# Optimization experiments

Measured on AMD Instinct MI355X. Metric: run time of the kernel, lower is better.

## Reference

```python
import jax, jax.numpy as jnp
import numpy as np

B, N, F_IN, H, E, C = 64, 1024, 128, 128, 1048576, 6
RATIO = 0.5
N1 = int(N * RATIO)        # nodes per graph after pool1 = 512
N2 = int(N1 * RATIO)       # nodes per graph after pool2 = 256


def setup_inputs() -> dict:
    key = jax.random.key(0)
    ks = jax.random.split(key, 14)
    x = jax.random.normal(ks[0], (B * N, F_IN), jnp.float32)
    # edges constrained within each graph (uniform graph size N)
    src = jax.random.randint(ks[1], (E,), 0, B * N, dtype=jnp.int32)
    dst = (src // N) * N + jax.random.randint(ks[2], (E,), 0, N, dtype=jnp.int32)
    edge_index = jnp.stack([src, dst]).astype(jnp.int64)
    batch = jnp.repeat(jnp.arange(B, dtype=jnp.int64), N)

    def lin(k, i, o):
        return (jax.random.normal(k, (i, o), jnp.float32) / np.sqrt(i)).astype(jnp.float32)

    W1 = lin(ks[3], F_IN, H); b1 = jnp.zeros((H,), jnp.float32)
    ws1 = jax.random.normal(ks[4], (H,), jnp.float32) / np.sqrt(H)
    W2 = lin(ks[5], H, H); b2 = jnp.zeros((H,), jnp.float32)
    ws2 = jax.random.normal(ks[6], (H,), jnp.float32) / np.sqrt(H)
    W3 = lin(ks[7], H, H); b3 = jnp.zeros((H,), jnp.float32)
    ws3 = jax.random.normal(ks[8], (H,), jnp.float32) / np.sqrt(H)
    L1w = lin(ks[9], 2 * H, H); L1b = jnp.zeros((H,), jnp.float32)
    L2w = lin(ks[10], H, H // 2); L2b = jnp.zeros((H // 2,), jnp.float32)
    L3w = lin(ks[11], H // 2, C); L3b = jnp.zeros((C,), jnp.float32)
    return dict(x=x, edge_index=edge_index, batch=batch,
                W1=W1, b1=b1, ws1=ws1, W2=W2, b2=b2, ws2=ws2, W3=W3, b3=b3, ws3=ws3,
                L1w=L1w, L1b=L1b, L2w=L2w, L2b=L2b, L3w=L3w, L3b=L3b)


def gcn_conv(x, src, dst, emask, W, b, ws, n_nodes):
    # GCNConv with self-loops: out_i = sum_j m_ij h_j / sqrt(d_i d_j) + h_i / d_i, d = deg+1
    h = x @ W
    deg = jax.ops.segment_sum(emask, dst, num_segments=n_nodes) + 1.0
    norm = emask / jnp.sqrt(deg[src] * deg[dst])                 # [E]
    agg = jax.ops.segment_sum(h[src] * norm[:, None], dst, num_segments=n_nodes)
    out = agg + h / deg[:, None] + b
    score = out @ ws                                             # [n] attention score
    return out, score


def att_pool(x, score, src, dst, emask, n_per_graph):
    # top-k node selection per graph (uniform sizes -> static shapes)
    k = int(n_per_graph * RATIO)
    vals, idx = jax.lax.top_k(score.reshape(B, n_per_graph), k)  # [B, k]
    gidx = (idx + (jnp.arange(B) * n_per_graph)[:, None]).reshape(-1)
    x_new = x[gidx] * jnp.tanh(vals.reshape(-1))[:, None]
    # remap old node ids -> new compact ids; drop edges touching removed nodes
    newpos = jnp.full((B * n_per_graph,), -1, jnp.int32).at[gidx].set(
        jnp.arange(B * k, dtype=jnp.int32))
    nsrc = newpos[src]; ndst = newpos[dst]
    nmask = emask * (nsrc >= 0) * (ndst >= 0)
    return x_new, jnp.maximum(nsrc, 0), jnp.maximum(ndst, 0), nmask, k


def readout(h, bvec, n_per_graph):
    gmp = jax.ops.segment_max(h, bvec, num_segments=B)
    gap = jax.ops.segment_sum(h, bvec, num_segments=B) / n_per_graph
    return jnp.concatenate([gmp, gap], axis=1)                   # [B, 2H]


def reference(x, edge_index, batch, W1, b1, ws1, W2, b2, ws2, W3, b3, ws3,
              L1w, L1b, L2w, L2b, L3w, L3b):
    src = edge_index[0].astype(jnp.int32)
    dst = edge_index[1].astype(jnp.int32)
    emask = jnp.ones((E,), x.dtype)

    h, s = gcn_conv(x, src, dst, emask, W1, b1, ws1, B * N)
    h = jax.nn.relu(h)
    h, src, dst, emask, k1 = att_pool(h, s, src, dst, emask, N)
    b1v = jnp.repeat(jnp.arange(B), k1)
    x1 = readout(h, b1v, float(k1))

    h, s = gcn_conv(h, src, dst, emask, W2, b2, ws2, B * k1)
    h = jax.nn.relu(h)
    h, src, dst, emask, k2 = att_pool(h, s, src, dst, emask, k1)
    b2v = jnp.repeat(jnp.arange(B), k2)
    x2 = readout(h, b2v, float(k2))

    h, s = gcn_conv(h, src, dst, emask, W3, b3, ws3, B * k2)
    h = jax.nn.relu(h)
    x3 = readout(h, b2v, float(k2))

    z = jax.nn.relu(x1) + jax.nn.relu(x2) + jax.nn.relu(x3)
    z = jax.nn.relu(z @ L1w + L1b)
    z = jax.nn.relu(z @ L2w + L2b)
    return jax.nn.log_softmax(z @ L3w + L3b, axis=-1)
```

## Files before the change

### kernel.cpp

```cpp
#include <hip/hip_runtime.h>
#include <math.h>

#define E_TOT 1048576
#define NB    64
#define HD    128
#define NN1   65536
#define NN2   32768
#define NN3   16384
#define CAP   18432
#define WST   140
#define PSTR  64

__global__ void probe_kernel(const int* __restrict__ ei, int* __restrict__ flag,
                             int* __restrict__ gcur, int2* __restrict__ csr2) {
    int t = threadIdx.x;
    if (t < 64) { gcur[t] = 0; csr2[E_TOT + t] = make_int2(0, 0); }
    if (blockIdx.x == 0 && t == 0) {
        int w = 1;
        for (int i = 1; i < 64; i += 2) if (ei[i] != 0) { w = 0; break; }
        *flag = w;
    }
}

__global__ __launch_bounds__(256) void bin_pack_kernel(const int* __restrict__ ei,
                                                       const int* __restrict__ wflag,
                                                       int* __restrict__ bins,
                                                       int* __restrict__ gcur) {
    __shared__ int hist[64];
    __shared__ int base[64];
    __shared__ int gpos[64];
    __shared__ int stage[4096];
    const int t = threadIdx.x;
    const int wide = *wflag;
    const int e0 = blockIdx.x * 4096;
    const int2* ei2 = (const int2*)ei;

    int pk[16];
    #pragma unroll
    for (int j = 0; j < 16; ++j) {
        int e = e0 + j * 256 + t;
        int s, d;
        if (wide) { s = ei2[e].x; d = ei2[E_TOT + e].x; }
        else      { s = ei[e];    d = ei[E_TOT + e]; }
        int g = d >> 10;
        pk[j] = (g << 20) | ((d & 1023) << 10) | (s & 1023);
    }
    if (t < 64) hist[t] = 0;
    __syncthreads();
    #pragma unroll
    for (int j = 0; j < 16; ++j) atomicAdd(&hist[pk[j] >> 20], 1);
    __syncthreads();
    if (t < 64) {
        int v = hist[t];
        int inc = v;
        #pragma unroll
        for (int d = 1; d < 64; d <<= 1) { int u = __shfl_up(inc, d); if (t >= d) inc += u; }
        base[t] = inc - v;
        gpos[t] = atomicAdd(&gcur[t], v);
    }
    __syncthreads();
    if (t < 64) hist[t] = base[t];
    __syncthreads();
    #pragma unroll
    for (int j = 0; j < 16; ++j) {
        int p = atomicAdd(&hist[pk[j] >> 20], 1);
        stage[p] = pk[j];
    }
    __syncthreads();
    #pragma unroll
    for (int j = 0; j < 16; ++j) {
        int i = j * 256 + t;
        int v = stage[i];
        int g = v >> 20;
        int dst = gpos[g] + (i - base[g]);
        if (dst < CAP) bins[g * CAP + dst] = v;
    }
}

__global__ __launch_bounds__(1024) void graph_csr_kernel(const int* __restrict__ bins,
                                                         const int* __restrict__ gcur,
                                                         int2* __restrict__ off2,
                                                         float* __restrict__ rs,
                                                         int2* __restrict__ csr2,
                                                         int* __restrict__ perm) {
    __shared__ int   deg[1024];
    __shared__ int   cur[1024];
    __shared__ float rsl[1024];
    __shared__ int   wsum[16];
    __shared__ int   dh[64];
    __shared__ int   dc[64];
    __shared__ int   ebase_s;
    const int g = blockIdx.x, t = threadIdx.x;
    const int lane = t & 63, wv = t >> 6;

    if (t < 64) {
        int v = gcur[t];
        int inc = v;
        #pragma unroll
        for (int d = 1; d < 64; d <<= 1) { int u = __shfl_up(inc, d); if (t >= d) inc += u; }
        if (t == g) ebase_s = inc - v;
    }
    deg[t] = 0;
    if (t < 64) dh[t] = 0;
    __syncthreads();
    const int cnt = gcur[g];
    const int ebase = ebase_s;
    const int* bin = bins + g * CAP;

    for (int i = t; i < cnt; i += 1024)
        atomicAdd(&deg[(bin[i] >> 10) & 1023], 1);
    __syncthreads();

    int dv = deg[t];
    int dcap = dv < 63 ? dv : 63;
    atomicAdd(&dh[dcap], 1);
    int inc = dv;
    #pragma unroll
    for (int d = 1; d < 64; d <<= 1) { int u = __shfl_up(inc, d); if (lane >= d) inc += u; }
    if (lane == 63) wsum[wv] = inc;
    __syncthreads();
    if (t < 16) {
        int v = wsum[t];
        int inc2 = v;
        #pragma unroll
        for (int d = 1; d < 16; d <<= 1) { int u = __shfl_up(inc2, d); if (t >= d) inc2 += u; }
        wsum[t] = inc2 - v;
    }
    if (t >= 64 && t < 128) {
        int l2 = t - 64;
        int v2 = dh[l2];
        int inc3 = v2;
        #pragma unroll
        for (int d = 1; d < 64; d <<= 1) { int u = __shfl_up(inc3, d); if (l2 >= d) inc3 += u; }
        dc[l2] = inc3 - v2;
    }
    __syncthreads();
    int ex = inc - dv + wsum[wv];
    int beg = ebase + ex;
    off2[g * 1024 + t] = make_int2(beg, beg + dv);
    float rv = rsqrtf((float)(dv + 1));
    rs[g * 1024 + t] = rv;
    rsl[t] = rv;
    cur[t] = ex;
    int r2 = atomicAdd(&dc[dcap], 1);
    perm[g * 1024 + r2] = t;
    __syncthreads();

    for (int i = t; i < cnt; i += 1024) {
        int v = bin[i];
        int s = v & 1023;
        int d = (v >> 10) & 1023;
        int p = atomicAdd(&cur[d], 1);
        csr2[ebase + p] = make_int2((g << 10) + s, __float_as_int(rsl[s] * rsl[d]));
    }
}

__global__ __launch_bounds__(256) void csr_build_kernel(const int2* __restrict__ old_off2,
                                                        const int* __restrict__ old_deg,
                                                        const int* __restrict__ old_csr,
                                                        int old_stride,
                                                        const int* __restrict__ map,
                                                        const int* __restrict__ sel,
                                                        int* __restrict__ new_csr,
                                                        int* __restrict__ deg,
                                                        float* __restrict__ rs, int nnew) {
    int wid  = (blockIdx.x * blockDim.x + threadIdx.x) >> 6;
    int lane = threadIdx.x & 63;
    if (wid >= nnew) return;
    int old = sel[wid];
    int beg, end;
    if (old_off2) { int2 oe = old_off2[old]; beg = oe.x; end = oe.y; }
    else          { beg = old * PSTR; end = beg + old_deg[old]; }
    int out = wid * PSTR;
    int total = 0;
    for (int base = beg; base < end; base += 64) {
        int i = base + lane;
        int ns = -1;
        if (i < end) ns = map[old_csr[i * old_stride]];
        unsigned long long b = __ballot(ns >= 0);
        int pos = __popcll(b & ((1ULL << lane) - 1));
        if (ns >= 0 && total + pos < PSTR) new_csr[out + total + pos] = ns;
        total += __popcll(b);
    }
    if (total > PSTR) total = PSTR;
    if (lane == 0) {
        deg[wid] = total;
        rs[wid]  = rsqrtf((float)(total + 1));
    }
}

__global__ __launch_bounds__(256) void gemm_tiled_kernel(const float* __restrict__ X,
                                                         const float* __restrict__ W,
                                                         float* __restrict__ Y) {
    __shared__ float sXT[2][16][128];
    __shared__ float sW[2][16][WST];
    const int t = threadIdx.x;
    const long long row0 = (long long)blockIdx.x * 128;
    const int r0 = (t >> 4) << 3;
    const int c0 = (t & 15) << 3;
    const int wofs = c0 + ((c0 >> 5) << 2);
    const int lm  = t >> 1;
    const int lk  = (t & 1) << 3;
    const int wk  = t >> 4;
    const int wc8 = (t & 15) << 3;
    const int wpos = wc8 + ((wc8 >> 5) << 2);

    float acc[8][8];
    #pragma unroll
    for (int i = 0; i < 8; ++i)
        #pragma unroll
        for (int j = 0; j < 8; ++j) acc[i][j] = 0.f;

    {
        float4 xa = *(const float4*)(X + (row0 + lm) * 128 + lk);
        float4 xb = *(const float4*)(X + (row0 + lm) * 128 + lk + 4);
        float4 wa = *(const float4*)(W + wk * 128 + wc8);
        float4 wb = *(const float4*)(W + wk * 128 + wc8 + 4);
        sXT[0][lk + 0][lm] = xa.x; sXT[0][lk + 1][lm] = xa.y;
        sXT[0][lk + 2][lm] = xa.z; sXT[0][lk + 3][lm] = xa.w;
        sXT[0][lk + 4][lm] = xb.x; sXT[0][lk + 5][lm] = xb.y;
        sXT[0][lk + 6][lm] = xb.z; sXT[0][lk + 7][lm] = xb.w;
        *(float4*)&sW[0][wk][wpos]     = wa;
        *(float4*)&sW[0][wk][wpos + 4] = wb;
    }
    int cur = 0;
    for (int k0 = 0; k0 < 128; k0 += 16) {
        __syncthreads();
        const bool hasNext = (k0 + 16) < 128;
        float4 nxa, nxb, nwa, nwb;
        if (hasNext) {
            nxa = *(const float4*)(X + (row0 + lm) * 128 + k0 + 16 + lk);
            nxb = *(const float4*)(X + (row0 + lm) * 128 + k0 + 16 + lk + 4);
            nwa = *(const float4*)(W + (k0 + 16 + wk) * 128 + wc8);
            nwb = *(const float4*)(W + (k0 + 16 + wk) * 128 + wc8 + 4);
        }
        #pragma unroll
        for (int kk = 0; kk < 16; ++kk) {
            float4 xa = *(const float4*)&sXT[cur][kk][r0];
            float4 xb = *(const float4*)&sXT[cur][kk][r0 + 4];
            float4 wa = *(const float4*)&sW[cur][kk][wofs];
            float4 wb = *(const float4*)&sW[cur][kk][wofs + 4];
            float xr[8]  = {xa.x, xa.y, xa.z, xa.w, xb.x, xb.y, xb.z, xb.w};
            float wcv[8] = {wa.x, wa.y, wa.z, wa.w, wb.x, wb.y, wb.z, wb.w};
            #pragma unroll
            for (int i = 0; i < 8; ++i)
                #pragma unroll
                for (int j = 0; j < 8; ++j)
                    acc[i][j] = fmaf(xr[i], wcv[j], acc[i][j]);
        }
        if (hasNext) {
            int nxt = cur ^ 1;
            sXT[nxt][lk + 0][lm] = nxa.x; sXT[nxt][lk + 1][lm] = nxa.y;
            sXT[nxt][lk + 2][lm] = nxa.z; sXT[nxt][lk + 3][lm] = nxa.w;
            sXT[nxt][lk + 4][lm] = nxb.x; sXT[nxt][lk + 5][lm] = nxb.y;
            sXT[nxt][lk + 6][lm] = nxb.z; sXT[nxt][lk + 7][lm] = nxb.w;
            *(float4*)&sW[nxt][wk][wpos]     = nwa;
            *(float4*)&sW[nxt][wk][wpos + 4] = nwb;
            cur = nxt;
        }
    }

    #pragma unroll
    for (int i = 0; i < 8; ++i) {
        float* yp = Y + (row0 + r0 + i) * 128 + c0;
        float4 o0; o0.x = acc[i][0]; o0.y = acc[i][1]; o0.z = acc[i][2]; o0.w = acc[i][3];
        float4 o1; o1.x = acc[i][4]; o1.y = acc[i][5]; o1.z = acc[i][6]; o1.w = acc[i][7];
        *(float4*)yp       = o0;
        *(float4*)(yp + 4) = o1;
    }
}

__global__ __launch_bounds__(256) void gemm_gather_kernel(const float* __restrict__ H,
                                                          const int* __restrict__ sel,
                                                          const float* __restrict__ scal,
                                                          const float* __restrict__ W,
                                                          float* __restrict__ Y) {
    __shared__ float sXT[2][16][128];
    __shared__ float sW[2][16][WST];
    const int t = threadIdx.x;
    const long long row0 = (long long)blockIdx.x * 128;
    const int r0 = (t >> 4) << 3;
    const int c0 = (t & 15) << 3;
    const int wofs = c0 + ((c0 >> 5) << 2);
    const int lm  = t >> 1;
    const int lk  = (t & 1) << 3;
    const int wk  = t >> 4;
    const int wc8 = (t & 15) << 3;
    const int wpos = wc8 + ((wc8 >> 5) << 2);

    const float* xrow = H + (long long)sel[row0 + lm] * 128;
    const float  sc   = scal[row0 + lm];

    float acc[8][8];
    #pragma unroll
    for (int i = 0; i < 8; ++i)
        #pragma unroll
        for (int j = 0; j < 8; ++j) acc[i][j] = 0.f;

    {
        float4 xa = *(const float4*)(xrow + lk);
        float4 xb = *(const float4*)(xrow + lk + 4);
        float4 wa = *(const float4*)(W + wk * 128 + wc8);
        float4 wb = *(const float4*)(W + wk * 128 + wc8 + 4);
        sXT[0][lk + 0][lm] = xa.x * sc; sXT[0][lk + 1][lm] = xa.y * sc;
        sXT[0][lk + 2][lm] = xa.z * sc; sXT[0][lk + 3][lm] = xa.w * sc;
        sXT[0][lk + 4][lm] = xb.x * sc; sXT[0][lk + 5][lm] = xb.y * sc;
        sXT[0][lk + 6][lm] = xb.z * sc; sXT[0][lk + 7][lm] = xb.w * sc;
        *(float4*)&sW[0][wk][wpos]     = wa;
        *(float4*)&sW[0][wk][wpos + 4] = wb;
    }
    int cur = 0;
    for (int k0 = 0; k0 < 128; k0 += 16) {
        __syncthreads();
        const bool hasNext = (k0 + 16) < 128;
        float4 nxa, nxb, nwa, nwb;
        if (hasNext) {
            nxa = *(const float4*)(xrow + k0 + 16 + lk);
            nxb = *(const float4*)(xrow + k0 + 16 + lk + 4);
            nwa = *(const float4*)(W + (k0 + 16 + wk) * 128 + wc8);
            nwb = *(const float4*)(W + (k0 + 16 + wk) * 128 + wc8 + 4);
        }
        #pragma unroll
        for (int kk = 0; kk < 16; ++kk) {
            float4 xa = *(const float4*)&sXT[cur][kk][r0];
            float4 xb = *(const float4*)&sXT[cur][kk][r0 + 4];
            float4 wa = *(const float4*)&sW[cur][kk][wofs];
            float4 wb = *(const float4*)&sW[cur][kk][wofs + 4];
            float xr[8]  = {xa.x, xa.y, xa.z, xa.w, xb.x, xb.y, xb.z, xb.w};
            float wcv[8] = {wa.x, wa.y, wa.z, wa.w, wb.x, wb.y, wb.z, wb.w};
            #pragma unroll
            for (int i = 0; i < 8; ++i)
                #pragma unroll
                for (int j = 0; j < 8; ++j)
                    acc[i][j] = fmaf(xr[i], wcv[j], acc[i][j]);
        }
        if (hasNext) {
            int nxt = cur ^ 1;
            sXT[nxt][lk + 0][lm] = nxa.x * sc; sXT[nxt][lk + 1][lm] = nxa.y * sc;
            sXT[nxt][lk + 2][lm] = nxa.z * sc; sXT[nxt][lk + 3][lm] = nxa.w * sc;
            sXT[nxt][lk + 4][lm] = nxb.x * sc; sXT[nxt][lk + 5][lm] = nxb.y * sc;
            sXT[nxt][lk + 6][lm] = nxb.z * sc; sXT[nxt][lk + 7][lm] = nxb.w * sc;
            *(float4*)&sW[nxt][wk][wpos]     = nwa;
            *(float4*)&sW[nxt][wk][wpos + 4] = nwb;
            cur = nxt;
        }
    }

    #pragma unroll
    for (int i = 0; i < 8; ++i) {
        float* yp = Y + (row0 + r0 + i) * 128 + c0;
        float4 o0; o0.x = acc[i][0]; o0.y = acc[i][1]; o0.z = acc[i][2]; o0.w = acc[i][3];
        float4 o1; o1.x = acc[i][4]; o1.y = acc[i][5]; o1.z = acc[i][6]; o1.w = acc[i][7];
        *(float4*)yp       = o0;
        *(float4*)(yp + 4) = o1;
    }
}

__global__ __launch_bounds__(1024) void agg_lds_kernel(const float* __restrict__ h,
                                                       const int2* __restrict__ csr2,
                                                       const int2* __restrict__ off2,
                                                       const float* __restrict__ rs,
                                                       const int* __restrict__ perm,
                                                       const float* __restrict__ bias,
                                                       const float* __restrict__ ws,
                                                       float* __restrict__ hrelu,
                                                       float* __restrict__ P) {
    __shared__ float sh[1024 * 36];
    const int t  = threadIdx.x;
    const int g  = blockIdx.x & 63;
    const int fc = blockIdx.x >> 6;
    const int nbase = g << 10;
    const float* hg = h + (size_t)nbase * 128 + fc * 32;

    #pragma unroll
    for (int it = 0; it < 8; ++it) {
        int i = it * 1024 + t;
        int r = i >> 3, p = i & 7;
        float4 v4 = *(const float4*)(hg + (size_t)r * 128 + p * 4);
        *(float4*)&sh[r * 36 + p * 4] = v4;
    }
    __syncthreads();

    const int q   = t & 7;
    const int grp = t >> 3;
    const int qb  = q << 2;

    float4 bb = *(const float4*)(bias + fc * 32 + qb);
    float4 ww = *(const float4*)(ws   + fc * 32 + qb);

    for (int pass = 0; pass < 8; ++pass) {
        int lv = perm[nbase + pass * 128 + grp];
        int v  = nbase + lv;
        int2 oe = off2[v];
        int beg = oe.x, end = oe.y;
        float rv = rs[v];
        float a0 = 0.f, a1 = 0.f, a2 = 0.f, a3 = 0.f;

        int2 er = csr2[beg + q];
        for (int eb = beg; eb < end; eb += 8) {
            int2 ern = csr2[eb + 8 + q];
            #pragma unroll
            for (int j = 0; j < 8; ++j) {
                int   sj = __shfl(er.x, j, 8);
                float nr = __int_as_float(__shfl(er.y, j, 8));
                float nj = (eb + j < end) ? nr : 0.f;
                const float4 e = *(const float4*)&sh[(sj & 1023) * 36 + qb];
                a0 = fmaf(e.x, nj, a0); a1 = fmaf(e.y, nj, a1);
                a2 = fmaf(e.z, nj, a2); a3 = fmaf(e.w, nj, a3);
            }
            er = ern;
        }

        float4 hv = *(const float4*)&sh[lv * 36 + qb];
        float inv = rv * rv;
        float o0 = a0 + hv.x * inv + bb.x;
        float o1 = a1 + hv.y * inv + bb.y;
        float o2 = a2 + hv.z * inv + bb.z;
        float o3 = a3 + hv.w * inv + bb.w;

        float pa = o0 * ww.x + o1 * ww.y;
        float pb = o2 * ww.z + o3 * ww.w;
        *(float2*)(P + (size_t)v * 64 + (fc * 8 + q) * 2) = make_float2(pa, pb);

        float4 o;
        o.x = fmaxf(o0, 0.f); o.y = fmaxf(o1, 0.f);
        o.z = fmaxf(o2, 0.f); o.w = fmaxf(o3, 0.f);
        *(float4*)(hrelu + (size_t)v * 128 + fc * 32 + qb) = o;
    }
}

__global__ __launch_bounds__(256) void score1_kernel(const float* __restrict__ P,
                                                     float* __restrict__ score) {
    int v = blockIdx.x * 256 + threadIdx.x;
    const float* buf = P + (size_t)v * 64;
    float a[32], b[32];
    #pragma unroll
    for (int i2 = 0; i2 < 16; ++i2) {
        float4 v4 = *(const float4*)(buf + i2 * 4);
        a[i2 * 2]     = v4.x; b[i2 * 2]     = v4.y;
        a[i2 * 2 + 1] = v4.z; b[i2 * 2 + 1] = v4.w;
    }
    float ua[16], ub[16];
    #pragma unroll
    for (int l = 0; l < 16; ++l) { ua[l] = a[l] + a[l + 16]; ub[l] = b[l] + b[l + 16]; }
    float va[8], vb[8];
    #pragma unroll
    for (int l = 0; l < 8; ++l) { va[l] = ua[l] + ua[l + 8]; vb[l] = ub[l] + ub[l + 8]; }
    float wa[4], wb[4];
    #pragma unroll
    for (int l = 0; l < 4; ++l) { wa[l] = va[l] + va[l + 4]; wb[l] = vb[l] + vb[l + 4]; }
    float xa0 = wa[0] + wa[2], xa1 = wa[1] + wa[3];
    float xb0 = wb[0] + wb[2], xb1 = wb[1] + wb[3];
    score[v] = (xa0 + xa1) + (xb0 + xb1);
}

__global__ __launch_bounds__(256) void agg_kernel(const float* __restrict__ h,
                                                  const int* __restrict__ csr,
                                                  const int2* __restrict__ off2,
                                                  const int* __restrict__ degp,
                                                  const float* __restrict__ rs,
                                                  const float* __restrict__ bias,
                                                  const float* __restrict__ ws,
                                                  float* __restrict__ hrelu,
                                                  float* __restrict__ score,
                                                  int npg, int lbshift, int padded) {
    const int lane = threadIdx.x & 63;
    const int wvb  = threadIdx.x >> 6;
    const int half = lane >> 5;
    const int li   = lane & 31;
    int b   = blockIdx.x;
    int xcd = b & 7;
    int i   = b >> 3;
    int gi  = i >> lbshift;
    int lb  = i & ((1 << lbshift) - 1);
    int g   = xcd + (gi << 3);
    int v   = g * npg + (lb << 3) + (wvb << 1) + half;

    int beg, end;
    if (padded) { beg = v * PSTR; end = beg + degp[v]; }
    else        { int2 oe = off2[v]; beg = oe.x; end = oe.y; }
    float rv = rs[v];
    const float4* h4 = (const float4*)h;
    float ax = 0.f, ay = 0.f, az = 0.f, aw = 0.f;

    for (int base = beg; base < end; base += 32) {
        int idx = base + li;
        int sv = (idx < end) ? csr[idx] : 0;
        int m = end - base; if (m > 32) m = 32;
        int j = 0;
        for (; j + 8 <= m; j += 8) {
            int s0 = __shfl(sv, j,     32);
            int s1 = __shfl(sv, j + 1, 32);
            int s2 = __shfl(sv, j + 2, 32);
            int s3 = __shfl(sv, j + 3, 32);
            int s4 = __shfl(sv, j + 4, 32);
            int s5 = __shfl(sv, j + 5, 32);
            int s6 = __shfl(sv, j + 6, 32);
            int s7 = __shfl(sv, j + 7, 32);
            float n0 = rs[s0] * rv, n1 = rs[s1] * rv, n2 = rs[s2] * rv, n3 = rs[s3] * rv;
            float n4 = rs[s4] * rv, n5 = rs[s5] * rv, n6 = rs[s6] * rv, n7 = rs[s7] * rv;
            float4 v0 = h4[(long long)s0 * 32 + li];
            float4 v1 = h4[(long long)s1 * 32 + li];
            float4 v2 = h4[(long long)s2 * 32 + li];
            float4 v3 = h4[(long long)s3 * 32 + li];
            float4 v4 = h4[(long long)s4 * 32 + li];
            float4 v5 = h4[(long long)s5 * 32 + li];
            float4 v6 = h4[(long long)s6 * 32 + li];
            float4 v7 = h4[(long long)s7 * 32 + li];
            ax = fmaf(v0.x, n0, ax); ay = fmaf(v0.y, n0, ay); az = fmaf(v0.z, n0, az); aw = fmaf(v0.w, n0, aw);
            ax = fmaf(v1.x, n1, ax); ay = fmaf(v1.y, n1, ay); az = fmaf(v1.z, n1, az); aw = fmaf(v1.w, n1, aw);
            ax = fmaf(v2.x, n2, ax); ay = fmaf(v2.y, n2, ay); az = fmaf(v2.z, n2, az); aw = fmaf(v2.w, n2, aw);
            ax = fmaf(v3.x, n3, ax); ay = fmaf(v3.y, n3, ay); az = fmaf(v3.z, n3, az); aw = fmaf(v3.w, n3, aw);
            ax = fmaf(v4.x, n4, ax); ay = fmaf(v4.y, n4, ay); az = fmaf(v4.z, n4, az); aw = fmaf(v4.w, n4, aw);
            ax = fmaf(v5.x, n5, ax); ay = fmaf(v5.y, n5, ay); az = fmaf(v5.z, n5, az); aw = fmaf(v5.w, n5, aw);
            ax = fmaf(v6.x, n6, ax); ay = fmaf(v6.y, n6, ay); az = fmaf(v6.z, n6, az); aw = fmaf(v6.w, n6, aw);
            ax = fmaf(v7.x, n7, ax); ay = fmaf(v7.y, n7, ay); az = fmaf(v7.z, n7, az); aw = fmaf(v7.w, n7, aw);
        }
        for (; j < m; ++j) {
            int s = __shfl(sv, j, 32);
            float n = rs[s] * rv;
            float4 vv = h4[(long long)s * 32 + li];
            ax = fmaf(vv.x, n, ax); ay = fmaf(vv.y, n, ay);
            az = fmaf(vv.z, n, az); aw = fmaf(vv.w, n, aw);
        }
    }

    float4 hv = h4[(long long)v * 32 + li];
    float inv = rv * rv;
    float4 bb = ((const float4*)bias)[li];
    float4 ww = ((const float4*)ws)[li];
    float o0 = ax + hv.x * inv + bb.x;
    float o1 = ay + hv.y * inv + bb.y;
    float o2 = az + hv.z * inv + bb.z;
    float o3 = aw + hv.w * inv + bb.w;

    float pa = o0 * ww.x + o1 * ww.y;
    float pb = o2 * ww.z + o3 * ww.w;
    #pragma unroll
    for (int dd = 16; dd; dd >>= 1) {
        pa += __shfl_xor(pa, dd, 32);
        pb += __shfl_xor(pb, dd, 32);
    }
    float p = pa + pb;
    if (li == 0) score[v] = p;

    float4 o;
    o.x = fmaxf(o0, 0.f); o.y = fmaxf(o1, 0.f);
    o.z = fmaxf(o2, 0.f); o.w = fmaxf(o3, 0.f);
    ((float4*)hrelu)[(long long)v * 32 + li] = o;
}

__global__ __launch_bounds__(1024) void topk_kernel(const float* __restrict__ score,
                                                    int* __restrict__ newpos,
                                                    int* __restrict__ sel,
                                                    float* __restrict__ scale,
                                                    int n, int k) {
    __shared__ float key[1024];
    __shared__ int   kid[1024];
    int g = blockIdx.x, t = threadIdx.x;
    key[t] = score[g * n + t];
    kid[t] = t;
    __syncthreads();
    for (int kk = 2; kk <= n; kk <<= 1) {
        for (int j = kk >> 1; j > 0; j >>= 1) {
            int ixj = t ^ j;
            if (ixj > t) {
                bool dir = ((t & kk) == 0);
                float a = key[t], b = key[ixj];
                if ((a < b) == dir) {
                    key[t] = b; key[ixj] = a;
                    int tmp = kid[t]; kid[t] = kid[ixj]; kid[ixj] = tmp;
                }
            }
            __syncthreads();
        }
    }
    int old = g * n + kid[t];
    if (t < k) {
        int nid = g * k + t;
        newpos[old] = nid;
        sel[nid]    = old;
        scale[nid]  = tanhf(key[t]);
    } else {
        newpos[old] = -1;
    }
}

__global__ __launch_bounds__(128) void readout_part_kernel(const float* __restrict__ h,
                                                           float* __restrict__ part, int npg) {
    int b = blockIdx.x;
    int g = b >> 3, c = b & 7;
    int f = threadIdx.x;
    int chunk = npg >> 3;
    const float* base = h + ((long long)g * npg + (long long)c * chunk) * 128;
    float m = -INFINITY, s = 0.f;
    for (int n = 0; n < chunk; ++n) {
        float v = base[n * 128 + f];
        m = fmaxf(m, v);
        s += v;
    }
    part[(size_t)b * 256 + f]       = m;
    part[(size_t)b * 256 + 128 + f] = s;
}

__global__ __launch_bounds__(128) void readout_gpart_kernel(const float* __restrict__ h,
                                                            const int* __restrict__ sel,
                                                            const float* __restrict__ scal,
                                                            float* __restrict__ part, int npg) {
    int b = blockIdx.x;
    int g = b >> 3, c = b & 7;
    int f = threadIdx.x;
    int chunk = npg >> 3;
    int i0 = g * npg + c * chunk;
    float m = -INFINITY, s = 0.f;
    for (int n = 0; n < chunk; ++n) {
        int idx = i0 + n;
        float v = h[(long long)sel[idx] * 128 + f] * scal[idx];
        m = fmaxf(m, v);
        s += v;
    }
    part[(size_t)b * 256 + f]       = m;
    part[(size_t)b * 256 + 128 + f] = s;
}

__global__ __launch_bounds__(128) void mlp_kernel(const float* __restrict__ part1,
                                                  const float* __restrict__ part2,
                                                  const float* __restrict__ part3,
                                                  const float* __restrict__ L1w,
                                                  const float* __restrict__ L1b,
                                                  const float* __restrict__ L2w,
                                                  const float* __restrict__ L2b,
                                                  const float* __restrict__ L3w,
                                                  const float* __restrict__ L3b,
                                                  float* __restrict__ out) {
    __shared__ float z[256], z1[128], z2[64], z3[6];
    int g = blockIdx.x, t = threadIdx.x;
    float m1 = -INFINITY, s1 = 0.f, m2 = -INFINITY, s2 = 0.f, m3 = -INFINITY, s3 = 0.f;
    #pragma unroll
    for (int c = 0; c < 8; ++c) {
        size_t o = (size_t)(g * 8 + c) * 256;
        m1 = fmaxf(m1, part1[o + t]); s1 += part1[o + 128 + t];
        m2 = fmaxf(m2, part2[o + t]); s2 += part2[o + 128 + t];
        m3 = fmaxf(m3, part3[o + t]); s3 += part3[o + 128 + t];
    }
    z[t]       = fmaxf(m1, 0.f) + fmaxf(m2, 0.f) + fmaxf(m3, 0.f);
    z[t + 128] = fmaxf(s1 / 512.f, 0.f) + fmaxf(s2 / 256.f, 0.f) + fmaxf(s3 / 256.f, 0.f);
    __syncthreads();
    float a = L1b[t];
    for (int i = 0; i < 256; ++i) a += z[i] * L1w[i * 128 + t];
    z1[t] = fmaxf(a, 0.f);
    __syncthreads();
    if (t < 64) {
        float b = L2b[t];
        for (int i = 0; i < 128; ++i) b += z1[i] * L2w[i * 64 + t];
        z2[t] = fmaxf(b, 0.f);
    }
    __syncthreads();
    if (t < 6) {
        float c = L3b[t];
        for (int i = 0; i < 64; ++i) c += z2[i] * L3w[i * 6 + t];
        z3[t] = c;
    }
    __syncthreads();
    if (t == 0) {
        float m = z3[0];
        for (int i = 1; i < 6; ++i) m = fmaxf(m, z3[i]);
        float s = 0.f;
        for (int i = 0; i < 6; ++i) s += expf(z3[i] - m);
        float ls = m + logf(s);
        for (int i = 0; i < 6; ++i) out[g * 6 + i] = z3[i] - ls;
    }
}

extern "C" void kernel_launch(void* const* d_in, const int* in_sizes, int n_in,
                              void* d_out, int out_size, void* d_ws, size_t ws_size,
                              hipStream_t stream) {
    const float* x    = (const float*)d_in[0];
    const int*   ei   = (const int*)d_in[1];
    const float* W1   = (const float*)d_in[3];
    const float* b1   = (const float*)d_in[4];
    const float* ws1  = (const float*)d_in[5];
    const float* W2   = (const float*)d_in[6];
    const float* b2   = (const float*)d_in[7];
    const float* ws2  = (const float*)d_in[8];
    const float* W3   = (const float*)d_in[9];
    const float* b3   = (const float*)d_in[10];
    const float* ws3  = (const float*)d_in[11];
    const float* L1w  = (const float*)d_in[12];
    const float* L1b  = (const float*)d_in[13];
    const float* L2w  = (const float*)d_in[14];
    const float* L2b  = (const float*)d_in[15];
    const float* L3w  = (const float*)d_in[16];
    const float* L3b  = (const float*)d_in[17];
    float* out = (float*)d_out;

    char* w = (char*)d_ws;
    auto alloc = [&](size_t nbytes) { char* p = w; w += (nbytes + 255) & ~(size_t)255; return p; };
    float* A     = (float*)alloc((size_t)NN1 * 128 * 4);
    float* Bf    = (float*)alloc((size_t)NN1 * 128 * 4);
    float* P1    = (float*)alloc((size_t)NN1 * 64 * 4);
    float* P2    = (float*)alloc((size_t)NN3 * 128 * 4);
    int2*  csr2  = (int2*)alloc((size_t)(E_TOT + 64) * 8);
    int*   degA  = (int*)alloc((size_t)NN2 * 4);
    int*   degB  = (int*)alloc((size_t)NN3 * 4);
    int2*  off2A = (int2*)alloc((size_t)NN1 * 8);
    float* rs    = (float*)alloc((size_t)NN1 * 4);
    int*   perm  = (int*)alloc((size_t)NN1 * 4);
    int*   np1   = (int*)alloc((size_t)NN1 * 4);
    int*   np2   = (int*)alloc((size_t)NN2 * 4);
    int*   sel   = (int*)alloc((size_t)NN2 * 4);
    float* scal  = (float*)alloc((size_t)NN2 * 4);
    float* score = (float*)alloc((size_t)NN1 * 4);
    float* part1 = (float*)alloc((size_t)NB * 8 * 256 * 4);
    float* part2 = (float*)alloc((size_t)NB * 8 * 256 * 4);
    float* part3 = (float*)alloc((size_t)NB * 8 * 256 * 4);
    int*   gcur  = (int*)alloc(64 * 4);
    int*   flag  = (int*)alloc(256);

    int*   bins = (int*)P2;
    float* Pp   = P1;
    int*   csrB = (int*)P1;
    int*   csrC = (int*)csr2;

    probe_kernel<<<1, 64, 0, stream>>>(ei, flag, gcur, csr2);

    bin_pack_kernel<<<E_TOT / 4096, 256, 0, stream>>>(ei, flag, bins, gcur);
    graph_csr_kernel<<<NB, 1024, 0, stream>>>(bins, gcur, off2A, rs, csr2, perm);
    gemm_tiled_kernel<<<NN1 / 128, 256, 0, stream>>>(x, W1, A);
    agg_lds_kernel<<<256, 1024, 0, stream>>>(A, csr2, off2A, rs, perm, b1, ws1, Bf, Pp);
    score1_kernel<<<NN1 / 256, 256, 0, stream>>>(Pp, score);
    topk_kernel<<<NB, 1024, 0, stream>>>(score, np1, sel, scal, 1024, 512);
    readout_gpart_kernel<<<NB * 8, 128, 0, stream>>>(Bf, sel, scal, part1, 512);

    csr_build_kernel<<<NN2 / 4, 256, 0, stream>>>(off2A, nullptr, (const int*)csr2, 2,
                                                  np1, sel, csrB, degA, rs, NN2);
    gemm_gather_kernel<<<NN2 / 128, 256, 0, stream>>>(Bf, sel, scal, W2, A);
    agg_kernel<<<NN2 / 8, 256, 0, stream>>>(A, csrB, nullptr, degA, rs, b2, ws2,
                                            Bf, score, 512, 6, 1);
    topk_kernel<<<NB, 512, 0, stream>>>(score, np2, sel, scal, 512, 256);
    readout_gpart_kernel<<<NB * 8, 128, 0, stream>>>(Bf, sel, scal, part2, 256);

    csr_build_kernel<<<NN3 / 4, 256, 0, stream>>>(nullptr, degA, csrB, 1,
                                                  np2, sel, csrC, degB, rs, NN3);
    gemm_gather_kernel<<<NN3 / 128, 256, 0, stream>>>(Bf, sel, scal, W3, A);
    agg_kernel<<<NN3 / 8, 256, 0, stream>>>(A, csrC, nullptr, degB, rs, b3, ws3,
                                            Bf, score, 256, 5, 1);
    readout_part_kernel<<<NB * 8, 128, 0, stream>>>(Bf, part3, 256);

    mlp_kernel<<<NB, 128, 0, stream>>>(part1, part2, part3, L1w, L1b, L2w, L2b,
                                       L3w, L3b, out);
}
```

Baseline: 360.0 us.

## Fuse independent stage kernels into block-partitioned launches and simplify edge loop

Merges independent kernels into single launches that dispatch on block index: bin packing plus the first GEMM, and per-stage gather-GEMM, CSR rebuild and readout. Shared memory is now dynamic and carved per role. This removes several kernel launches and the serialization between independent work, so they can run concurrently on the GPU. The first-layer aggregation loop also drops the shuffle-based prefetch of edges in favour of direct loads with a separate tail, which may change memory latency hiding. The fused kernels use the largest role's shared memory and registers for every block, which could lower occupancy for the lighter roles.

```diff
diff --git a/kernel.cpp b/kernel.cpp
--- a/kernel.cpp
+++ b/kernel.cpp
@@ -10,6 +10,7 @@
 #define CAP   18432
 #define WST   140
 #define PSTR  64
+#define SMEM_PREP (2*16*128*4 + 2*16*WST*4)
 
 __global__ void probe_kernel(const int* __restrict__ ei, int* __restrict__ flag,
                              int* __restrict__ gcur, int2* __restrict__ csr2) {
@@ -22,17 +23,17 @@
     }
 }
 
-__global__ __launch_bounds__(256) void bin_pack_kernel(const int* __restrict__ ei,
-                                                       const int* __restrict__ wflag,
-                                                       int* __restrict__ bins,
-                                                       int* __restrict__ gcur) {
-    __shared__ int hist[64];
-    __shared__ int base[64];
-    __shared__ int gpos[64];
-    __shared__ int stage[4096];
+__device__ __forceinline__ void bin_pack_body(char* smem, const int* __restrict__ ei,
+                                              const int* __restrict__ wflag,
+                                              int* __restrict__ bins,
+                                              int* __restrict__ gcur, int bid) {
+    int* hist  = (int*)smem;
+    int* base  = hist + 64;
+    int* gpos  = base + 64;
+    int* stage = gpos + 64;
     const int t = threadIdx.x;
     const int wide = *wflag;
-    const int e0 = blockIdx.x * 4096;
+    const int e0 = bid * 4096;
     const int2* ei2 = (const int2*)ei;
 
     int pk[16];
@@ -75,6 +76,186 @@
         int dst = gpos[g] + (i - base[g]);
         if (dst < CAP) bins[g * CAP + dst] = v;
     }
+}
+
+__device__ __forceinline__ void gemm_body(char* smem, const float* __restrict__ X,
+                                          const int* __restrict__ sel,
+                                          const float* __restrict__ scal,
+                                          const float* __restrict__ W,
+                                          float* __restrict__ Y, int bid) {
+    float* sXT = (float*)smem;
+    float* sW  = sXT + 2 * 16 * 128;
+    const int t = threadIdx.x;
+    const long long row0 = (long long)bid * 128;
+    const int r0 = (t >> 4) << 3;
+    const int c0 = (t & 15) << 3;
+    const int wofs = c0 + ((c0 >> 5) << 2);
+    const int lm  = t >> 1;
+    const int lk  = (t & 1) << 3;
+    const int wk  = t >> 4;
+    const int wc8 = (t & 15) << 3;
+    const int wpos = wc8 + ((wc8 >> 5) << 2);
+
+    const float* xrow;
+    float sc;
+    if (sel) { xrow = X + (long long)sel[row0 + lm] * 128; sc = scal[row0 + lm]; }
+    else     { xrow = X + (row0 + lm) * 128;               sc = 1.f; }
+
+    float acc[8][8];
+    #pragma unroll
+    for (int i = 0; i < 8; ++i)
+        #pragma unroll
+        for (int j = 0; j < 8; ++j) acc[i][j] = 0.f;
+
+    {
+        float4 xa = *(const float4*)(xrow + lk);
+        float4 xb = *(const float4*)(xrow + lk + 4);
+        float4 wa = *(const float4*)(W + wk * 128 + wc8);
+        float4 wb = *(const float4*)(W + wk * 128 + wc8 + 4);
+        sXT[(lk + 0) * 128 + lm] = xa.x * sc; sXT[(lk + 1) * 128 + lm] = xa.y * sc;
+        sXT[(lk + 2) * 128 + lm] = xa.z * sc; sXT[(lk + 3) * 128 + lm] = xa.w * sc;
+        sXT[(lk + 4) * 128 + lm] = xb.x * sc; sXT[(lk + 5) * 128 + lm] = xb.y * sc;
+        sXT[(lk + 6) * 128 + lm] = xb.z * sc; sXT[(lk + 7) * 128 + lm] = xb.w * sc;
+        *(float4*)&sW[wk * WST + wpos]     = wa;
+        *(float4*)&sW[wk * WST + wpos + 4] = wb;
+    }
+    int cur = 0;
+    for (int k0 = 0; k0 < 128; k0 += 16) {
+        __syncthreads();
+        const bool hasNext = (k0 + 16) < 128;
+        float4 nxa, nxb, nwa, nwb;
+        if (hasNext) {
+            nxa = *(const float4*)(xrow + k0 + 16 + lk);
+            nxb = *(const float4*)(xrow + k0 + 16 + lk + 4);
+            nwa = *(const float4*)(W + (k0 + 16 + wk) * 128 + wc8);
+            nwb = *(const float4*)(W + (k0 + 16 + wk) * 128 + wc8 + 4);
+        }
+        #pragma unroll
+        for (int kk = 0; kk < 16; ++kk) {
+            float4 xa = *(const float4*)&sXT[(cur * 16 + kk) * 128 + r0];
+            float4 xb = *(const float4*)&sXT[(cur * 16 + kk) * 128 + r0 + 4];
+            float4 wa = *(const float4*)&sW[(cur * 16 + kk) * WST + wofs];
+            float4 wb = *(const float4*)&sW[(cur * 16 + kk) * WST + wofs + 4];
+            float xr[8]  = {xa.x, xa.y, xa.z, xa.w, xb.x, xb.y, xb.z, xb.w};
+            float wcv[8] = {wa.x, wa.y, wa.z, wa.w, wb.x, wb.y, wb.z, wb.w};
+            #pragma unroll
+            for (int i = 0; i < 8; ++i)
+                #pragma unroll
+                for (int j = 0; j < 8; ++j)
+                    acc[i][j] = fmaf(xr[i], wcv[j], acc[i][j]);
+        }
+        if (hasNext) {
+            int nxt = cur ^ 1;
+            sXT[(nxt * 16 + lk + 0) * 128 + lm] = nxa.x * sc;
+            sXT[(nxt * 16 + lk + 1) * 128 + lm] = nxa.y * sc;
+            sXT[(nxt * 16 + lk + 2) * 128 + lm] = nxa.z * sc;
+            sXT[(nxt * 16 + lk + 3) * 128 + lm] = nxa.w * sc;
+            sXT[(nxt * 16 + lk + 4) * 128 + lm] = nxb.x * sc;
+            sXT[(nxt * 16 + lk + 5) * 128 + lm] = nxb.y * sc;
+            sXT[(nxt * 16 + lk + 6) * 128 + lm] = nxb.z * sc;
+            sXT[(nxt * 16 + lk + 7) * 128 + lm] = nxb.w * sc;
+            *(float4*)&sW[(nxt * 16 + wk) * WST + wpos]     = nwa;
+            *(float4*)&sW[(nxt * 16 + wk) * WST + wpos + 4] = nwb;
+            cur = nxt;
+        }
+    }
+
+    #pragma unroll
+    for (int i = 0; i < 8; ++i) {
+        float* yp = Y + (row0 + r0 + i) * 128 + c0;
+        float4 o0; o0.x = acc[i][0]; o0.y = acc[i][1]; o0.z = acc[i][2]; o0.w = acc[i][3];
+        float4 o1; o1.x = acc[i][4]; o1.y = acc[i][5]; o1.z = acc[i][6]; o1.w = acc[i][7];
+        *(float4*)yp       = o0;
+        *(float4*)(yp + 4) = o1;
+    }
+}
+
+__device__ __forceinline__ void csr_build_body(const int2* __restrict__ old_off2,
+                                               const int* __restrict__ old_deg,
+                                               const int* __restrict__ old_csr,
+                                               int old_stride,
+                                               const int* __restrict__ map,
+                                               const int* __restrict__ sel,
+                                               int* __restrict__ new_csr,
+                                               int* __restrict__ deg,
+                                               float* __restrict__ rs,
+                                               int nnew, int wid, int lane) {
+    if (wid >= nnew) return;
+    int old = sel[wid];
+    int beg, end;
+    if (old_off2) { int2 oe = old_off2[old]; beg = oe.x; end = oe.y; }
+    else          { beg = old * PSTR; end = beg + old_deg[old]; }
+    int out = wid * PSTR;
+    int total = 0;
+    for (int base = beg; base < end; base += 64) {
+        int i = base + lane;
+        int ns = -1;
+        if (i < end) ns = map[old_csr[i * old_stride]];
+        unsigned long long b = __ballot(ns >= 0);
+        int pos = __popcll(b & ((1ULL << lane) - 1));
+        if (ns >= 0 && total + pos < PSTR) new_csr[out + total + pos] = ns;
+        total += __popcll(b);
+    }
+    if (total > PSTR) total = PSTR;
+    if (lane == 0) {
+        deg[wid] = total;
+        rs[wid]  = rsqrtf((float)(total + 1));
+    }
+}
+
+__device__ __forceinline__ void readout_g_body(const float* __restrict__ h,
+                                               const int* __restrict__ sel,
+                                               const float* __restrict__ scal,
+                                               float* __restrict__ part,
+                                               int npg, int b, int f) {
+    int g = b >> 3, c = b & 7;
+    int chunk = npg >> 3;
+    int i0 = g * npg + c * chunk;
+    float m = -INFINITY, s = 0.f;
+    for (int n = 0; n < chunk; ++n) {
+        int idx = i0 + n;
+        float v = h[(long long)sel[idx] * 128 + f] * scal[idx];
+        m = fmaxf(m, v);
+        s += v;
+    }
+    part[(size_t)b * 256 + f]       = m;
+    part[(size_t)b * 256 + 128 + f] = s;
+}
+
+__global__ __launch_bounds__(256) void prep1_kernel(const int* __restrict__ ei,
+                                                    const int* __restrict__ wflag,
+                                                    int* __restrict__ bins,
+                                                    int* __restrict__ gcur,
+                                                    const float* __restrict__ X,
+                                                    const float* __restrict__ W1,
+                                                    float* __restrict__ A) {
+    extern __shared__ __align__(16) char smem[];
+    if (blockIdx.x < 256) bin_pack_body(smem, ei, wflag, bins, gcur, blockIdx.x);
+    else                  gemm_body(smem, X, nullptr, nullptr, W1, A, blockIdx.x - 256);
+}
+
+__global__ __launch_bounds__(256) void stage_prep_kernel(
+        const float* __restrict__ Bf, const int* __restrict__ sel,
+        const float* __restrict__ scal, const float* __restrict__ W,
+        float* __restrict__ A,
+        const int2* __restrict__ old_off2, const int* __restrict__ old_deg,
+        const int* __restrict__ old_csr, int old_stride,
+        const int* __restrict__ map, int* __restrict__ new_csr,
+        int* __restrict__ deg, float* __restrict__ rs, int nnew,
+        float* __restrict__ part, int npg, int ngemm, int ncsr) {
+    extern __shared__ __align__(16) char smem[];
+    int b = blockIdx.x;
+    if (b < ngemm) { gemm_body(smem, Bf, sel, scal, W, A, b); return; }
+    b -= ngemm;
+    if (b < ncsr) {
+        csr_build_body(old_off2, old_deg, old_csr, old_stride, map, sel,
+                       new_csr, deg, rs, nnew, b * 4 + (threadIdx.x >> 6),
+                       threadIdx.x & 63);
+        return;
+    }
+    b -= ncsr;
+    readout_g_body(Bf, sel, scal, part, npg, b * 2 + (threadIdx.x >> 7),
+                   threadIdx.x & 127);
 }
 
 __global__ __launch_bounds__(1024) void graph_csr_kernel(const int* __restrict__ bins,
@@ -155,207 +336,6 @@
     }
 }
 
-__global__ __launch_bounds__(256) void csr_build_kernel(const int2* __restrict__ old_off2,
-                                                        const int* __restrict__ old_deg,
-                                                        const int* __restrict__ old_csr,
-                                                        int old_stride,
-                                                        const int* __restrict__ map,
-                                                        const int* __restrict__ sel,
-                                                        int* __restrict__ new_csr,
-                                                        int* __restrict__ deg,
-                                                        float* __restrict__ rs, int nnew) {
-    int wid  = (blockIdx.x * blockDim.x + threadIdx.x) >> 6;
-    int lane = threadIdx.x & 63;
-    if (wid >= nnew) return;
-    int old = sel[wid];
-    int beg, end;
-    if (old_off2) { int2 oe = old_off2[old]; beg = oe.x; end = oe.y; }
-    else          { beg = old * PSTR; end = beg + old_deg[old]; }
-    int out = wid * PSTR;
-    int total = 0;
-    for (int base = beg; base < end; base += 64) {
-        int i = base + lane;
-        int ns = -1;
-        if (i < end) ns = map[old_csr[i * old_stride]];
-        unsigned long long b = __ballot(ns >= 0);
-        int pos = __popcll(b & ((1ULL << lane) - 1));
-        if (ns >= 0 && total + pos < PSTR) new_csr[out + total + pos] = ns;
-        total += __popcll(b);
-    }
-    if (total > PSTR) total = PSTR;
-    if (lane == 0) {
-        deg[wid] = total;
-        rs[wid]  = rsqrtf((float)(total + 1));
-    }
-}
-
-__global__ __launch_bounds__(256) void gemm_tiled_kernel(const float* __restrict__ X,
-                                                         const float* __restrict__ W,
-                                                         float* __restrict__ Y) {
-    __shared__ float sXT[2][16][128];
-    __shared__ float sW[2][16][WST];
-    const int t = threadIdx.x;
-    const long long row0 = (long long)blockIdx.x * 128;
-    const int r0 = (t >> 4) << 3;
-    const int c0 = (t & 15) << 3;
-    const int wofs = c0 + ((c0 >> 5) << 2);
-    const int lm  = t >> 1;
-    const int lk  = (t & 1) << 3;
-    const int wk  = t >> 4;
-    const int wc8 = (t & 15) << 3;
-    const int wpos = wc8 + ((wc8 >> 5) << 2);
-
-    float acc[8][8];
-    #pragma unroll
-    for (int i = 0; i < 8; ++i)
-        #pragma unroll
-        for (int j = 0; j < 8; ++j) acc[i][j] = 0.f;
-
-    {
-        float4 xa = *(const float4*)(X + (row0 + lm) * 128 + lk);
-        float4 xb = *(const float4*)(X + (row0 + lm) * 128 + lk + 4);
-        float4 wa = *(const float4*)(W + wk * 128 + wc8);
-        float4 wb = *(const float4*)(W + wk * 128 + wc8 + 4);
-        sXT[0][lk + 0][lm] = xa.x; sXT[0][lk + 1][lm] = xa.y;
-        sXT[0][lk + 2][lm] = xa.z; sXT[0][lk + 3][lm] = xa.w;
-        sXT[0][lk + 4][lm] = xb.x; sXT[0][lk + 5][lm] = xb.y;
-        sXT[0][lk + 6][lm] = xb.z; sXT[0][lk + 7][lm] = xb.w;
-        *(float4*)&sW[0][wk][wpos]     = wa;
-        *(float4*)&sW[0][wk][wpos + 4] = wb;
-    }
-    int cur = 0;
-    for (int k0 = 0; k0 < 128; k0 += 16) {
-        __syncthreads();
-        const bool hasNext = (k0 + 16) < 128;
-        float4 nxa, nxb, nwa, nwb;
-        if (hasNext) {
-            nxa = *(const float4*)(X + (row0 + lm) * 128 + k0 + 16 + lk);
-            nxb = *(const float4*)(X + (row0 + lm) * 128 + k0 + 16 + lk + 4);
-            nwa = *(const float4*)(W + (k0 + 16 + wk) * 128 + wc8);
-            nwb = *(const float4*)(W + (k0 + 16 + wk) * 128 + wc8 + 4);
-        }
-        #pragma unroll
-        for (int kk = 0; kk < 16; ++kk) {
-            float4 xa = *(const float4*)&sXT[cur][kk][r0];
-            float4 xb = *(const float4*)&sXT[cur][kk][r0 + 4];
-            float4 wa = *(const float4*)&sW[cur][kk][wofs];
-            float4 wb = *(const float4*)&sW[cur][kk][wofs + 4];
-            float xr[8]  = {xa.x, xa.y, xa.z, xa.w, xb.x, xb.y, xb.z, xb.w};
-            float wcv[8] = {wa.x, wa.y, wa.z, wa.w, wb.x, wb.y, wb.z, wb.w};
-            #pragma unroll
-            for (int i = 0; i < 8; ++i)
-                #pragma unroll
-                for (int j = 0; j < 8; ++j)
-                    acc[i][j] = fmaf(xr[i], wcv[j], acc[i][j]);
-        }
-        if (hasNext) {
-            int nxt = cur ^ 1;
-            sXT[nxt][lk + 0][lm] = nxa.x; sXT[nxt][lk + 1][lm] = nxa.y;
-            sXT[nxt][lk + 2][lm] = nxa.z; sXT[nxt][lk + 3][lm] = nxa.w;
-            sXT[nxt][lk + 4][lm] = nxb.x; sXT[nxt][lk + 5][lm] = nxb.y;
-            sXT[nxt][lk + 6][lm] = nxb.z; sXT[nxt][lk + 7][lm] = nxb.w;
-            *(float4*)&sW[nxt][wk][wpos]     = nwa;
-            *(float4*)&sW[nxt][wk][wpos + 4] = nwb;
-            cur = nxt;
-        }
-    }
-
-    #pragma unroll
-    for (int i = 0; i < 8; ++i) {
-        float* yp = Y + (row0 + r0 + i) * 128 + c0;
-        float4 o0; o0.x = acc[i][0]; o0.y = acc[i][1]; o0.z = acc[i][2]; o0.w = acc[i][3];
-        float4 o1; o1.x = acc[i][4]; o1.y = acc[i][5]; o1.z = acc[i][6]; o1.w = acc[i][7];
-        *(float4*)yp       = o0;
-        *(float4*)(yp + 4) = o1;
-    }
-}
-
-__global__ __launch_bounds__(256) void gemm_gather_kernel(const float* __restrict__ H,
-                                                          const int* __restrict__ sel,
-                                                          const float* __restrict__ scal,
-                                                          const float* __restrict__ W,
-                                                          float* __restrict__ Y) {
-    __shared__ float sXT[2][16][128];
-    __shared__ float sW[2][16][WST];
-    const int t = threadIdx.x;
-    const long long row0 = (long long)blockIdx.x * 128;
-    const int r0 = (t >> 4) << 3;
-    const int c0 = (t & 15) << 3;
-    const int wofs = c0 + ((c0 >> 5) << 2);
-    const int lm  = t >> 1;
-    const int lk  = (t & 1) << 3;
-    const int wk  = t >> 4;
-    const int wc8 = (t & 15) << 3;
-    const int wpos = wc8 + ((wc8 >> 5) << 2);
-
-    const float* xrow = H + (long long)sel[row0 + lm] * 128;
-    const float  sc   = scal[row0 + lm];
-
-    float acc[8][8];
-    #pragma unroll
-    for (int i = 0; i < 8; ++i)
-        #pragma unroll
-        for (int j = 0; j < 8; ++j) acc[i][j] = 0.f;
-
-    {
-        float4 xa = *(const float4*)(xrow + lk);
-        float4 xb = *(const float4*)(xrow + lk + 4);
-        float4 wa = *(const float4*)(W + wk * 128 + wc8);
-        float4 wb = *(const float4*)(W + wk * 128 + wc8 + 4);
-        sXT[0][lk + 0][lm] = xa.x * sc; sXT[0][lk + 1][lm] = xa.y * sc;
-        sXT[0][lk + 2][lm] = xa.z * sc; sXT[0][lk + 3][lm] = xa.w * sc;
-        sXT[0][lk + 4][lm] = xb.x * sc; sXT[0][lk + 5][lm] = xb.y * sc;
-        sXT[0][lk + 6][lm] = xb.z * sc; sXT[0][lk + 7][lm] = xb.w * sc;
-        *(float4*)&sW[0][wk][wpos]     = wa;
-        *(float4*)&sW[0][wk][wpos + 4] = wb;
-    }
-    int cur = 0;
-    for (int k0 = 0; k0 < 128; k0 += 16) {
-        __syncthreads();
-        const bool hasNext = (k0 + 16) < 128;
-        float4 nxa, nxb, nwa, nwb;
-        if (hasNext) {
-            nxa = *(const float4*)(xrow + k0 + 16 + lk);
-            nxb = *(const float4*)(xrow + k0 + 16 + lk + 4);
-            nwa = *(const float4*)(W + (k0 + 16 + wk) * 128 + wc8);
-            nwb = *(const float4*)(W + (k0 + 16 + wk) * 128 + wc8 + 4);
-        }
-        #pragma unroll
-        for (int kk = 0; kk < 16; ++kk) {
-            float4 xa = *(const float4*)&sXT[cur][kk][r0];
-            float4 xb = *(const float4*)&sXT[cur][kk][r0 + 4];
-            float4 wa = *(const float4*)&sW[cur][kk][wofs];
-            float4 wb = *(const float4*)&sW[cur][kk][wofs + 4];
-            float xr[8]  = {xa.x, xa.y, xa.z, xa.w, xb.x, xb.y, xb.z, xb.w};
-            float wcv[8] = {wa.x, wa.y, wa.z, wa.w, wb.x, wb.y, wb.z, wb.w};
-            #pragma unroll
-            for (int i = 0; i < 8; ++i)
-                #pragma unroll
-                for (int j = 0; j < 8; ++j)
-                    acc[i][j] = fmaf(xr[i], wcv[j], acc[i][j]);
-        }
-        if (hasNext) {
-            int nxt = cur ^ 1;
-            sXT[nxt][lk + 0][lm] = nxa.x * sc; sXT[nxt][lk + 1][lm] = nxa.y * sc;
-            sXT[nxt][lk + 2][lm] = nxa.z * sc; sXT[nxt][lk + 3][lm] = nxa.w * sc;
-            sXT[nxt][lk + 4][lm] = nxb.x * sc; sXT[nxt][lk + 5][lm] = nxb.y * sc;
-            sXT[nxt][lk + 6][lm] = nxb.z * sc; sXT[nxt][lk + 7][lm] = nxb.w * sc;
-            *(float4*)&sW[nxt][wk][wpos]     = nwa;
-            *(float4*)&sW[nxt][wk][wpos + 4] = nwb;
-            cur = nxt;
-        }
-    }
-
-    #pragma unroll
-    for (int i = 0; i < 8; ++i) {
-        float* yp = Y + (row0 + r0 + i) * 128 + c0;
-        float4 o0; o0.x = acc[i][0]; o0.y = acc[i][1]; o0.z = acc[i][2]; o0.w = acc[i][3];
-        float4 o1; o1.x = acc[i][4]; o1.y = acc[i][5]; o1.z = acc[i][6]; o1.w = acc[i][7];
-        *(float4*)yp       = o0;
-        *(float4*)(yp + 4) = o1;
-    }
-}
-
 __global__ __launch_bounds__(1024) void agg_lds_kernel(const float* __restrict__ h,
                                                        const int2* __restrict__ csr2,
                                                        const int2* __restrict__ off2,
@@ -396,19 +376,26 @@
         float rv = rs[v];
         float a0 = 0.f, a1 = 0.f, a2 = 0.f, a3 = 0.f;
 
-        int2 er = csr2[beg + q];
-        for (int eb = beg; eb < end; eb += 8) {
-            int2 ern = csr2[eb + 8 + q];
+        int eb = beg;
+        for (; eb + 8 <= end; eb += 8) {
             #pragma unroll
             for (int j = 0; j < 8; ++j) {
-                int   sj = __shfl(er.x, j, 8);
-                float nr = __int_as_float(__shfl(er.y, j, 8));
-                float nj = (eb + j < end) ? nr : 0.f;
-                const float4 e = *(const float4*)&sh[(sj & 1023) * 36 + qb];
-                a0 = fmaf(e.x, nj, a0); a1 = fmaf(e.y, nj, a1);
-                a2 = fmaf(e.z, nj, a2); a3 = fmaf(e.w, nj, a3);
+                int2 e = csr2[eb + j];
+                float nj = __int_as_float(e.y);
+                const float4 hv4 = *(const float4*)&sh[(e.x & 1023) * 36 + qb];
+                a0 = fmaf(hv4.x, nj, a0); a1 = fmaf(hv4.y, nj, a1);
+                a2 = fmaf(hv4.z, nj, a2); a3 = fmaf(hv4.w, nj, a3);
             }
-            er = ern;
+        }
+        if (eb < end) {
+            #pragma unroll
+            for (int j = 0; j < 8; ++j) {
+                int2 e = csr2[eb + j];
+                float nj = (eb + j < end) ? __int_as_float(e.y) : 0.f;
+                const float4 hv4 = *(const float4*)&sh[(e.x & 1023) * 36 + qb];
+                a0 = fmaf(hv4.x, nj, a0); a1 = fmaf(hv4.y, nj, a1);
+                a2 = fmaf(hv4.z, nj, a2); a3 = fmaf(hv4.w, nj, a3);
+            }
         }
 
         float4 hv = *(const float4*)&sh[lv * 36 + qb];
@@ -603,26 +590,6 @@
     part[(size_t)b * 256 + 128 + f] = s;
 }
 
-__global__ __launch_bounds__(128) void readout_gpart_kernel(const float* __restrict__ h,
-                                                            const int* __restrict__ sel,
-                                                            const float* __restrict__ scal,
-                                                            float* __restrict__ part, int npg) {
-    int b = blockIdx.x;
-    int g = b >> 3, c = b & 7;
-    int f = threadIdx.x;
-    int chunk = npg >> 3;
-    int i0 = g * npg + c * chunk;
-    float m = -INFINITY, s = 0.f;
-    for (int n = 0; n < chunk; ++n) {
-        int idx = i0 + n;
-        float v = h[(long long)sel[idx] * 128 + f] * scal[idx];
-        m = fmaxf(m, v);
-        s += v;
-    }
-    part[(size_t)b * 256 + f]       = m;
-    part[(size_t)b * 256 + 128 + f] = s;
-}
-
 __global__ __launch_bounds__(128) void mlp_kernel(const float* __restrict__ part1,
                                                   const float* __restrict__ part2,
                                                   const float* __restrict__ part3,
@@ -724,25 +691,22 @@
 
     probe_kernel<<<1, 64, 0, stream>>>(ei, flag, gcur, csr2);
 
-    bin_pack_kernel<<<E_TOT / 4096, 256, 0, stream>>>(ei, flag, bins, gcur);
+    prep1_kernel<<<768, 256, SMEM_PREP, stream>>>(ei, flag, bins, gcur, x, W1, A);
     graph_csr_kernel<<<NB, 1024, 0, stream>>>(bins, gcur, off2A, rs, csr2, perm);
-    gemm_tiled_kernel<<<NN1 / 128, 256, 0, stream>>>(x, W1, A);
     agg_lds_kernel<<<256, 1024, 0, stream>>>(A, csr2, off2A, rs, perm, b1, ws1, Bf, Pp);
     score1_kernel<<<NN1 / 256, 256, 0, stream>>>(Pp, score);
     topk_kernel<<<NB, 1024, 0, stream>>>(score, np1, sel, scal, 1024, 512);
-    readout_gpart_kernel<<<NB * 8, 128, 0, stream>>>(Bf, sel, scal, part1, 512);
-
-    csr_build_kernel<<<NN2 / 4, 256, 0, stream>>>(off2A, nullptr, (const int*)csr2, 2,
-                                                  np1, sel, csrB, degA, rs, NN2);
-    gemm_gather_kernel<<<NN2 / 128, 256, 0, stream>>>(Bf, sel, scal, W2, A);
+
+    stage_prep_kernel<<<256 + NN2 / 4 + 256, 256, SMEM_PREP, stream>>>(
+        Bf, sel, scal, W2, A, off2A, nullptr, (const int*)csr2, 2,
+        np1, csrB, degA, rs, NN2, part1, 512, 256, NN2 / 4);
     agg_kernel<<<NN2 / 8, 256, 0, stream>>>(A, csrB, nullptr, degA, rs, b2, ws2,
                                             Bf, score, 512, 6, 1);
     topk_kernel<<<NB, 512, 0, stream>>>(score, np2, sel, scal, 512, 256);
-    readout_gpart_kernel<<<NB * 8, 128, 0, stream>>>(Bf, sel, scal, part2, 256);
-
-    csr_build_kernel<<<NN3 / 4, 256, 0, stream>>>(nullptr, degA, csrB, 1,
-                                                  np2, sel, csrC, degB, rs, NN3);
-    gemm_gather_kernel<<<NN3 / 128, 256, 0, stream>>>(Bf, sel, scal, W3, A);
+
+    stage_prep_kernel<<<128 + NN3 / 4 + 256, 256, SMEM_PREP, stream>>>(
+        Bf, sel, scal, W3, A, nullptr, degA, csrB, 1,
+        np2, csrC, degB, rs, NN3, part2, 256, 128, NN3 / 4);
     agg_kernel<<<NN3 / 8, 256, 0, stream>>>(A, csrC, nullptr, degB, rs, b3, ws3,
                                             Bf, score, 256, 5, 1);
     readout_part_kernel<<<NB * 8, 128, 0, stream>>>(Bf, part3, 256);
```

Result: no change. 357.4 us (-0.7%).
